# Kernel optimization log

Hardware: AMD Instinct MI355X
Metric: run time of the kernel (lower is better)

Reference implementation:

```python
import jax, jax.numpy as jnp
import numpy as np

B, S, D, NL = 512, 200, 128, 2
N_ITEMS = 50001
DH = 2 * D
DFF = 4 * D


def layer_norm(x, g, b, eps=1e-5):
    mu = x.mean(-1, keepdims=True)
    v = ((x - mu) ** 2).mean(-1, keepdims=True)
    return (x - mu) / jnp.sqrt(v + eps) * g + b


def lru_scan(h, lamb0, mask):
    # h: (B, L, DH) complex64, lamb0: (DH,) complex64, mask: (B, L) bool
    Bb, L, Dh = h.shape
    log2_L = int(np.ceil(np.log2(L)))
    lamb = lamb0.reshape(1, Dh)
    for i in range(1, log2_L + 1):
        l = 2 ** i
        h = h.reshape(Bb * L // l, l, Dh)
        m = mask.reshape(Bb * L // l, l)
        h1, h2 = h[:, : l // 2], h[:, l // 2:]
        if i > 1:
            lamb = jnp.concatenate([lamb, lamb * lamb[-1]], axis=0)  # powers lambda^1..lambda^(l/2)
        carry_gate = m[:, l // 2 - 1 : l // 2, None].astype(h.dtype)
        h2 = h2 + lamb * h1[:, -1:] * carry_gate
        h = jnp.concatenate([h1, h2], axis=1)
    return h.reshape(Bb, L, Dh)


def _forward(token_emb, emb_ln_g, emb_ln_b, params_log,
             in_wr, in_wi, in_br, in_bi, out_wr, out_wi, out_br, out_bi,
             lru_ln_g, lru_ln_b, w1, b1, w2, b2, ffn_ln_g, ffn_ln_b,
             item_seq, item_seq_len):
    mask = item_seq > 0                      # (B, S)
    x = token_emb[item_seq]                  # (B, S, D)
    x = layer_norm(x, emb_ln_g, emb_ln_b)
    seq_len = item_seq.shape[1]
    L = 2 ** int(np.ceil(np.log2(seq_len)))
    pad = L - seq_len
    x = jnp.pad(x, ((0, 0), (pad, 0), (0, 0)))        # left-pad seq to power of 2
    m = jnp.pad(mask, ((0, 0), (pad, 0)))
    n_layers = params_log.shape[0]
    for li in range(n_layers):
        pl = jnp.exp(params_log[li])                  # (3, DH): nu, theta, gamma
        nu, theta, gamma = pl[0], pl[1], pl[2]
        lamb0 = jnp.exp(jax.lax.complex(-nu, theta))  # (DH,)
        in_w = jax.lax.complex(in_wr[li], in_wi[li])
        in_b = jax.lax.complex(in_br[li], in_bi[li])
        h = (jnp.einsum('bld,hd->blh', x.astype(jnp.complex64), in_w) + in_b) * gamma
        h = lru_scan(h, lamb0, m)
        out_w = jax.lax.complex(out_wr[li], out_wi[li])
        out_b = jax.lax.complex(out_br[li], out_bi[li])
        y = (jnp.einsum('blh,dh->bld', h, out_w) + out_b).real + x
        x = layer_norm(y, lru_ln_g[li], lru_ln_b[li])
        # positionwise FFN with residual + post-LN
        hff = jax.nn.gelu(jnp.einsum('bld,fd->blf', x, w1[li]) + b1[li], approximate=False)
        x = layer_norm(jnp.einsum('blf,df->bld', hff, w2[li]) + b2[li] + x,
                       ffn_ln_g[li], ffn_ln_b[li])
    x = x[:, -seq_len:]                               # (B, S, D)
    idx = item_seq_len - 1
    return x[jnp.arange(x.shape[0]), idx]             # (B, D)


def setup_inputs() -> dict:
    key = jax.random.key(0)
    ks = jax.random.split(key, 24)
    std = 0.02
    item_seq = jax.random.randint(ks[0], (B, S), 0, N_ITEMS)
    item_seq_len = jax.random.randint(ks[1], (B,), 1, S + 1)
    # LRU diagonal init (matches torch init)
    r_min, r_max = 0.8, 0.99
    u1 = jax.random.uniform(ks[2], (NL, DH))
    u2 = jax.random.uniform(ks[3], (NL, DH))
    nu_log = jnp.log(-0.5 * jnp.log(u1 * (r_max ** 2 - r_min ** 2) + r_min ** 2))
    theta_log = jnp.log(u2 * 2.0 * np.pi)
    gamma_log = 0.5 * jnp.log(1.0 - jnp.exp(-2.0 * jnp.exp(nu_log)))
    params_log = jnp.stack([nu_log, theta_log, gamma_log], axis=1)  # (NL, 3, DH)
    rn = lambda k, sh: jax.random.normal(k, sh, dtype=jnp.float32) * std
    return {
        'token_emb': rn(ks[4], (N_ITEMS, D)),
        'emb_ln_g': jnp.ones((D,), jnp.float32), 'emb_ln_b': jnp.zeros((D,), jnp.float32),
        'params_log': params_log,
        'in_wr': rn(ks[5], (NL, DH, D)), 'in_wi': rn(ks[6], (NL, DH, D)),
        'in_br': rn(ks[7], (NL, DH)), 'in_bi': rn(ks[8], (NL, DH)),
        'out_wr': rn(ks[9], (NL, D, DH)), 'out_wi': rn(ks[10], (NL, D, DH)),
        'out_br': rn(ks[11], (NL, D)), 'out_bi': rn(ks[12], (NL, D)),
        'lru_ln_g': jnp.ones((NL, D), jnp.float32), 'lru_ln_b': jnp.zeros((NL, D), jnp.float32),
        'w1': rn(ks[13], (NL, DFF, D)), 'b1': rn(ks[14], (NL, DFF)),
        'w2': rn(ks[15], (NL, D, DFF)), 'b2': rn(ks[16], (NL, D)),
        'ffn_ln_g': jnp.ones((NL, D), jnp.float32), 'ffn_ln_b': jnp.zeros((NL, D), jnp.float32),
        'item_seq': item_seq, 'item_seq_len': item_seq_len,
    }


def reference(token_emb, emb_ln_g, emb_ln_b, params_log,
              in_wr, in_wi, in_br, in_bi, out_wr, out_wi, out_br, out_bi,
              lru_ln_g, lru_ln_b, w1, b1, w2, b2, ffn_ln_g, ffn_ln_b,
              item_seq, item_seq_len):
    return _forward(token_emb, emb_ln_g, emb_ln_b, params_log,
                    in_wr, in_wi, in_br, in_bi, out_wr, out_wi, out_br, out_bi,
                    lru_ln_g, lru_ln_b, w1, b1, w2, b2, ffn_ln_g, ffn_ln_b,
                    item_seq, item_seq_len)
```

## Files before the change

### kernel.cpp

```cpp
#include <hip/hip_runtime.h>
#include <hip/hip_bf16.h>
#include <math.h>

#define B_TOT 512
#define SEQ   200
#define D     128
#define DH    256
#define DFF   512
#define LPAD  256
#define PADL  56
#define NLAY  2
#define SST   18

typedef __attribute__((ext_vector_type(8))) short bf16x8;
typedef __attribute__((ext_vector_type(4))) float floatx4;

static __device__ inline float bf2f(ushort u) {
    union { unsigned int i; float f; } v; v.i = ((unsigned int)u) << 16; return v.f;
}
static __device__ inline ushort f2bf(float x) {
    union { float f; unsigned int i; } v; v.f = x;
    unsigned int r = (v.i + 0x7FFFu + ((v.i >> 16) & 1u)) >> 16;
    return (ushort)r;
}
static __device__ inline unsigned int pkbf(float a, float b) {
    union { __hip_bfloat162 h; unsigned int u; } v;
    v.h = __float22bfloat162_rn(make_float2(a, b));
    return v.u;
}
static __device__ inline void gld_lds16(const void* g, void* l) {
    __builtin_amdgcn_global_load_lds(
        (const __attribute__((address_space(1))) unsigned int*)g,
        (__attribute__((address_space(3))) unsigned int*)l, 16, 0, 0);
}

static __device__ inline size_t haddr(int b, int s, int k) {
    int p  = k >> 8;
    int ch = k & 255;
    int g  = ch >> 5;
    int cl = ch & 31;
    return (((((size_t)b * 8 + g) * 2 + p) * SEQ + s) * 32 + cl);
}

__global__ void setup_all_kernel(const float* __restrict__ params_log,
                                 const float* __restrict__ in_br,
                                 const float* __restrict__ in_bi,
                                 const float* __restrict__ in_wr,
                                 const float* __restrict__ in_wi,
                                 const float* __restrict__ out_wr,
                                 const float* __restrict__ out_wi,
                                 const float* __restrict__ w1,
                                 const float* __restrict__ w2,
                                 ushort* __restrict__ Winb,
                                 ushort* __restrict__ W2effb,
                                 ushort* __restrict__ w1b,
                                 ushort* __restrict__ w2b,
                                 float* __restrict__ lam_pow,
                                 float* __restrict__ scale_in,
                                 float* __restrict__ bias_in)
{
    int idx = blockIdx.x * blockDim.x + threadIdx.x;
    int li = idx >> 16;
    int e  = idx & 65535;

    {
        int gp = e >> 12, rem = e & 4095;
        int q = rem >> 3, e8 = rem & 7;
        int r = q >> 4, cs = q & 15;
        int c16 = cs ^ (r & 7);
        int n = (r < 16) ? (gp * 16 + r) : (256 + gp * 16 + (r - 16));
        int d = c16 * 8 + e8;
        float wv = (n < DH) ? in_wr[((size_t)li * DH + n) * D + d]
                            : in_wi[((size_t)li * DH + (n - DH)) * D + d];
        Winb[idx] = f2bf(wv);
    }
    {
        int k0c = e >> 13, rem = e & 8191;
        int q = rem >> 3, e8 = rem & 7;
        int r = q >> 3, cs = q & 7;
        int c16 = cs ^ (r & 7);
        int k = k0c * 64 + c16 * 8 + e8;
        float w2v = (k < DH) ? out_wr[((size_t)li * D + r) * DH + k]
                             : -out_wi[((size_t)li * D + r) * DH + (k - DH)];
        W2effb[idx] = f2bf(w2v);
    }
    {
        int row = e >> 7, col = e & 127;
        int ffc = row >> 7, rl = row & 127;
        int c16 = col >> 3, e8 = col & 7;
        int cs = c16 ^ (rl & 7);
        w1b[li * 65536 + ffc * 16384 + rl * 128 + cs * 8 + e8] = f2bf(w1[idx]);
    }
    {
        int dd2 = e >> 9, kk = e & 511;
        int ffc = kk >> 7, klc = kk & 127;
        int c16 = klc >> 3, e8 = klc & 7;
        int cs = c16 ^ (dd2 & 7);
        w2b[li * 65536 + ffc * 16384 + dd2 * 128 + cs * 8 + e8] = f2bf(w2[idx]);
    }

    if (blockIdx.x < NLAY) {
        int pli = blockIdx.x;
        int c = threadIdx.x;
        const float* pl = params_log + (size_t)pli * 3 * DH;
        float nu = expf(pl[c]);
        float th = expf(pl[DH + c]);
        float ga = expf(pl[2 * DH + c]);
        float mag = expf(-nu);
        float lr = mag * cosf(th);
        float lim = mag * sinf(th);
        float2* lp = (float2*)(lam_pow + (size_t)pli * 65536) + (size_t)c * 128;
        float pr = lr, pi = lim;
        lp[0] = make_float2(pr, pi);
        for (int k = 1; k < 128; ++k) {
            float nr = pr * lr - pi * lim;
            float ni = pr * lim + pi * lr;
            pr = nr; pi = ni;
            lp[k] = make_float2(pr, pi);
        }
        scale_in[pli * 2 * DH + c]      = ga;
        scale_in[pli * 2 * DH + DH + c] = ga;
        bias_in[pli * 2 * DH + c]       = in_br[pli * DH + c] * ga;
        bias_in[pli * 2 * DH + DH + c]  = in_bi[pli * DH + c] * ga;
    }
}

__global__ __launch_bounds__(512) void build_rowmap_kernel(
    const int* __restrict__ lenp, int Bc,
    int* __restrict__ total, int* __restrict__ rowmap)
{
    __shared__ int pre[513];
    int tid = threadIdx.x;
    int lv = (tid < Bc) ? lenp[tid] : 0;
    pre[tid + 1] = lv;
    if (tid == 0) pre[0] = 0;
    __syncthreads();
    for (int ofs = 1; ofs < 512; ofs <<= 1) {
        int v = pre[tid + 1];
        int vv = (tid + 1 > ofs) ? pre[tid + 1 - ofs] : 0;
        __syncthreads();
        pre[tid + 1] = v + vv;
        __syncthreads();
    }
    if (tid == 0) total[0] = pre[Bc];
    if (tid < Bc) {
        int base = pre[tid];
        int n = lv;
        int rb = tid * SEQ;
        for (int s = 0; s < n; ++s) rowmap[base + s] = rb + s;
    }
}

__global__ __launch_bounds__(256) void embed_ln_kernel(
    const float* __restrict__ emb, const int* __restrict__ seq,
    const int* __restrict__ lenp,
    const float* __restrict__ g, const float* __restrict__ bt,
    ushort* __restrict__ x)
{
    int row  = blockIdx.x * 4 + (threadIdx.x >> 6);
    int lane = threadIdx.x & 63;
    int b = row / SEQ, s = row - b * SEQ;
    if (s >= lenp[b]) return;
    int item = seq[row];
    float2 v = *(const float2*)(emb + (size_t)item * D + lane * 2);
    float ssum = v.x + v.y;
#pragma unroll
    for (int o = 32; o > 0; o >>= 1) ssum += __shfl_xor(ssum, o);
    float mu = ssum * (1.0f / D);
    float d0 = v.x - mu, d1 = v.y - mu;
    float vs = d0 * d0 + d1 * d1;
#pragma unroll
    for (int o = 32; o > 0; o >>= 1) vs += __shfl_xor(vs, o);
    float rstd = rsqrtf(vs * (1.0f / D) + 1e-5f);
    float2 gg = *(const float2*)(g + lane * 2);
    float2 bb = *(const float2*)(bt + lane * 2);
    unsigned int o2 = pkbf(d0 * rstd * gg.x + bb.x, d1 * rstd * gg.y + bb.y);
    *(unsigned int*)(x + (size_t)row * D + lane * 2) = o2;
}

template <bool LAST>
__global__ __launch_bounds__(512) void inproj_scan_kernel(
    const ushort* __restrict__ X, const ushort* __restrict__ Win,
    ushort* __restrict__ H, const float2* __restrict__ lamT,
    const int* __restrict__ seq, const int* __restrict__ lenp,
    const float* __restrict__ scale_in, const float* __restrict__ bias_in)
{
    __shared__ __align__(16) char smem[36864];
    __shared__ float mkf[LPAD];
    char*  Wsm = smem;
    char*  xs  = smem + 8192;
    float* stR = (float*)smem;
    float* stI = stR + LPAD * SST;
    float2* lamS = (float2*)smem;
    float2* bc   = (float2*)(smem + 16 * 130 * 8);

    int gp = blockIdx.x, b = blockIdx.y;
    int tid = threadIdx.x;
    int l = tid & 63, w = tid >> 6;
    int ct = w & 1;
    int rq = w >> 1;
    int lr = l & 15, lq = l >> 4;
    int wbase = tid & ~63;

    int c  = tid & 15;
    int tl = tid >> 4;
    int t0 = tl * 8;

    int s_b = lenp[b] - 1;
    int tile_max = s_b >> 4;
    int nrows = (tile_max + 1) * 16;
    int tb = s_b + PADL;

    const float2* myl = lamT + (size_t)(gp * 16 + c) * 128;
    float2 l14[4];
#pragma unroll
    for (int k = 0; k < 4; ++k) l14[k] = myl[k];

    if (tid < LPAD) {
        int t = tid;
        float m = 0.f;
        if (t >= PADL) m = (seq[(size_t)b * SEQ + (t - PADL)] > 0) ? 1.f : 0.f;
        mkf[t] = m;
    }

    const ushort* xrow = X + (size_t)b * SEQ * 128;
    gld_lds16(Win + (size_t)gp * 4096 + (size_t)tid * 8,
              Wsm + (size_t)wbase * 16);
#pragma unroll
    for (int it = 0; it < 4; ++it) {
        int idx = it * 512 + tid;
        if (idx < 112 * 16) {
            int r = idx >> 4, c16 = idx & 15;
            if (r < nrows) {
                uint4 v = *(const uint4*)(xrow + (size_t)r * 128 + c16 * 8);
                *(uint4*)(xs + r * 256 + ((c16 ^ (r & 7)) * 16)) = v;
            }
        }
    }
    __syncthreads();

    bf16x8 wf[4];
#pragma unroll
    for (int kk = 0; kk < 4; ++kk) {
        int ca = kk * 4 + lq;
        int wr = ct * 16 + lr;
        wf[kk] = *(const bf16x8*)(Wsm + wr * 256 + ((ca ^ (wr & 7)) * 16));
    }
    int tstart = rq ? (3 * rq + 1) : 0;
    int tcnt   = rq ? 3 : 4;
    floatx4 acc[4];
#pragma unroll
    for (int tt = 0; tt < 4; ++tt) acc[tt] = (floatx4)0.f;

    if (rq < 2) {
#pragma unroll
        for (int tt = 0; tt < 4; ++tt) {
            if (tt < tcnt && (tstart + tt) <= tile_max) {
                int t  = tstart + tt;
                int ar = t * 16 + lr;
#pragma unroll
                for (int kk = 0; kk < 4; ++kk) {
                    int ca = kk * 4 + lq;
                    bf16x8 af = *(const bf16x8*)(xs + ar * 256 + ((ca ^ (ar & 7)) * 16));
                    acc[tt] = __builtin_amdgcn_mfma_f32_16x16x32_bf16(wf[kk], af, acc[tt], 0, 0, 0);
                }
            }
        }
    }
    __syncthreads();

    if (nrows > 112) {
#pragma unroll
        for (int it = 0; it < 3; ++it) {
            int idx = it * 512 + tid;
            int r = idx >> 4, c16 = idx & 15;
            int gr = 112 + r;
            if (gr < nrows) {
                uint4 v = make_uint4(0u, 0u, 0u, 0u);
                if (gr < 200) v = *(const uint4*)(xrow + (size_t)gr * 128 + c16 * 8);
                *(uint4*)(xs + r * 256 + ((c16 ^ (r & 7)) * 16)) = v;
            }
        }
    }
    __syncthreads();

    if (rq >= 2) {
#pragma unroll
        for (int tt = 0; tt < 4; ++tt) {
            if (tt < tcnt && (tstart + tt) <= tile_max) {
                int t  = tstart + tt;
                int ar = (t - 7) * 16 + lr;
#pragma unroll
                for (int kk = 0; kk < 4; ++kk) {
                    int ca = kk * 4 + lq;
                    bf16x8 af = *(const bf16x8*)(xs + ar * 256 + ((ca ^ (ar & 7)) * 16));
                    acc[tt] = __builtin_amdgcn_mfma_f32_16x16x32_bf16(wf[kk], af, acc[tt], 0, 0, 0);
                }
            }
        }
    }
    __syncthreads();

    for (int idx = tid; idx < PADL * SST; idx += 512) { stR[idx] = 0.f; stI[idx] = 0.f; }
    {
        float4 g4 = *(const float4*)(scale_in + ct * 256 + gp * 16 + lq * 4);
        float4 b4 = *(const float4*)(bias_in  + ct * 256 + gp * 16 + lq * 4);
        float* dst = ct ? stI : stR;
#pragma unroll
        for (int tt = 0; tt < 4; ++tt) {
            if (tt < tcnt && (tstart + tt) <= tile_max) {
                int t = tstart + tt;
                int s = t * 16 + lr;
                if (s <= s_b) {
                    int pos = s + PADL;
                    dst[pos * SST + lq * 4 + 0] = acc[tt][0] * g4.x + b4.x;
                    dst[pos * SST + lq * 4 + 1] = acc[tt][1] * g4.y + b4.y;
                    dst[pos * SST + lq * 4 + 2] = acc[tt][2] * g4.z + b4.z;
                    dst[pos * SST + lq * 4 + 3] = acc[tt][3] * g4.w + b4.w;
                }
            }
        }
    }
    __syncthreads();

    float xr[8], xi[8], mf[8];
#pragma unroll
    for (int k = 0; k < 8; ++k) {
        xr[k] = stR[(t0 + k) * SST + c];
        xi[k] = stI[(t0 + k) * SST + c];
        mf[k] = mkf[t0 + k];
    }
    __syncthreads();

    {
        const char* src = (const char*)(lamT + (size_t)gp * 16 * 128);
#pragma unroll
        for (int it = 0; it < 2; ++it) {
            int idx = it * 512 + tid;
            int row = idx >> 6, c4 = idx & 63;
            *(uint4*)((char*)lamS + row * 1040 + c4 * 16) =
                *(const uint4*)(src + row * 1024 + c4 * 16);
        }
    }

    if (t0 <= tb) {
#pragma unroll
        for (int k = 0; k < 8; k += 2) {
            float sr = xr[k] * mf[k], si = xi[k] * mf[k];
            xr[k+1] += l14[0].x * sr - l14[0].y * si;
            xi[k+1] += l14[0].x * si + l14[0].y * sr;
        }
#pragma unroll
        for (int k = 1; k < 8; k += 4) {
            float sr = xr[k] * mf[k], si = xi[k] * mf[k];
            xr[k+1] += l14[0].x * sr - l14[0].y * si;
            xi[k+1] += l14[0].x * si + l14[0].y * sr;
            xr[k+2] += l14[1].x * sr - l14[1].y * si;
            xi[k+2] += l14[1].x * si + l14[1].y * sr;
        }
        {
            float sr = xr[3] * mf[3], si = xi[3] * mf[3];
#pragma unroll
            for (int j = 0; j < 4; ++j) {
                xr[4+j] += l14[j].x * sr - l14[j].y * si;
                xi[4+j] += l14[j].x * si + l14[j].y * sr;
            }
        }
    }

#pragma unroll
    for (int i = 4; i <= 8; ++i) {
        int half = 1 << (i - 1);
        if (half > tb) continue;
        int buf  = (i & 1) * 544;
        bc[buf + tl * 17 + c] = make_float2(xr[7], xi[7]);
        __syncthreads();
        int off = t0 & ((half << 1) - 1);
        if (off >= half && t0 <= tb) {
            int src = t0 - off + half - 1;
            float m = mkf[src];
            float2 sv = bc[buf + (src >> 3) * 17 + c];
            float sr = sv.x * m, si = sv.y * m;
            int e = off - half;
            const float2* lp = lamS + c * 130 + e;
#pragma unroll
            for (int k = 0; k < 8; ++k) {
                float2 lv = lp[k];
                xr[k] += lv.x * sr - lv.y * si;
                xi[k] += lv.x * si + lv.y * sr;
            }
        }
    }
    __syncthreads();

#pragma unroll
    for (int k = 0; k < 8; ++k) {
        stR[(t0 + k) * SST + c] = xr[k];
        stI[(t0 + k) * SST + c] = xi[k];
    }
    __syncthreads();

    if (LAST) {
        if (tid < 32) {
            int t = tb;
            int p = tid >> 4, cc = tid & 15;
            float v = (p ? stI : stR)[t * SST + cc];
            H[(size_t)b * 512 + p * 256 + gp * 16 + cc] = f2bf(v);
        }
    } else {
        int g  = gp >> 1;
        int hc = (gp & 1) * 16;
        ushort* baseg = H + (size_t)(b * 8 + g) * 2 * SEQ * 32 + hc;
#pragma unroll
        for (int it = 0; it < 4; ++it) {
            int idx4 = it * 512 + tid;
            if (idx4 < 2 * SEQ * 4) {
                int q  = idx4 & 3;
                int ps = idx4 >> 2;
                int p  = ps >= SEQ;
                int s  = ps - p * SEQ;
                if (s > s_b) continue;
                int t  = s + PADL;
                const float* sp = (p ? stI : stR) + t * SST + q * 4;
                float2 a = *(const float2*)(sp);
                float2 d = *(const float2*)(sp + 2);
                uint2 raw;
                raw.x = pkbf(a.x, a.y);
                raw.y = pkbf(d.x, d.y);
                *(uint2*)(baseg + (size_t)ps * 32 + q * 4) = raw;
            }
        }
    }
}

__global__ __launch_bounds__(512) void outproj_kernel(
    const ushort* __restrict__ A, const ushort* __restrict__ Wimg,
    ushort* __restrict__ Cout,
    const int* __restrict__ rowmap, const int* __restrict__ totalp,
    const float* __restrict__ e0,
    const ushort* __restrict__ res,
    const float* __restrict__ lng, const float* __restrict__ lnb)
{
    int m0 = blockIdx.x * 256;
    int total = totalp[0];
    if (m0 >= total) return;
    __shared__ __align__(16) char As[32768];
    __shared__ __align__(16) char Bs[16384];
    __shared__ float2 lnS[2][256];
    int tid = threadIdx.x;
    int l = tid & 63, w = tid >> 6;
    int chh = w >> 2;
    int rh  = w & 3;
    int lr = l & 15, lq = l >> 4;
    int wbase = tid & ~63;

    int cst = tid & 7;
    int rr  = tid >> 3;
    int sb[4], ss[4];
#pragma unroll
    for (int it = 0; it < 4; ++it) {
        int gr = m0 + it * 64 + rr;
        if (gr >= total) gr = total - 1;
        int rm = rowmap[gr];
        sb[it] = rm / SEQ; ss[it] = rm - sb[it] * SEQ;
    }

    floatx4 acc[4][4];
#pragma unroll
    for (int i = 0; i < 4; ++i)
#pragma unroll
        for (int j = 0; j < 4; ++j) acc[i][j] = (floatx4)0.f;

    for (int k0c = 0; k0c < 8; ++k0c) {
        int k0 = k0c * 64;
        {
            const ushort* img = Wimg + (size_t)k0c * 8192;
#pragma unroll
            for (int it = 0; it < 2; ++it)
                gld_lds16(img + (size_t)(it * 512 + tid) * 8,
                          Bs + (size_t)(it * 512 + wbase) * 16);
        }
#pragma unroll
        for (int it = 0; it < 4; ++it) {
            int r = it * 64 + rr;
            uint4 va = *(const uint4*)(A + haddr(sb[it], ss[it], k0 + cst * 8));
            *(uint4*)(As + r * 128 + ((cst ^ (r & 7)) * 16)) = va;
        }
        __syncthreads();
#pragma unroll
        for (int kk = 0; kk < 2; ++kk) {
            bf16x8 wf[4], af[4];
            int ca = kk * 4 + lq;
#pragma unroll
            for (int i = 0; i < 4; ++i) {
                int rb = chh * 64 + i * 16 + lr;
                wf[i] = *(const bf16x8*)(Bs + rb * 128 + ((ca ^ (rb & 7)) * 16));
                int ra = rh * 64 + i * 16 + lr;
                af[i] = *(const bf16x8*)(As + ra * 128 + ((ca ^ (ra & 7)) * 16));
            }
#pragma unroll
            for (int i = 0; i < 4; ++i)
#pragma unroll
                for (int j = 0; j < 4; ++j)
                    acc[i][j] = __builtin_amdgcn_mfma_f32_16x16x32_bf16(
                        wf[i], af[j], acc[i][j], 0, 0, 0);
        }
        __syncthreads();
    }

    int chb[4], arow[4], rmj[4];
#pragma unroll
    for (int i = 0; i < 4; ++i) chb[i] = chh * 64 + i * 16 + lq * 4;
#pragma unroll
    for (int j = 0; j < 4; ++j) {
        arow[j] = m0 + rh * 64 + j * 16 + lr;
        int rc = arow[j] < total ? arow[j] : total - 1;
        rmj[j] = rowmap[rc];
    }

    {
        float4 bias[4], gv[4], bv[4];
#pragma unroll
        for (int i = 0; i < 4; ++i) {
            bias[i] = *(const float4*)(e0 + chb[i]);
            gv[i]   = *(const float4*)(lng + chb[i]);
            bv[i]   = *(const float4*)(lnb + chb[i]);
        }
#pragma unroll
        for (int j = 0; j < 4; ++j) {
#pragma unroll
            for (int i = 0; i < 4; ++i) {
                ushort4 r4 = *(const ushort4*)(res + (size_t)rmj[j] * 128 + chb[i]);
                acc[i][j][0] += ((const float*)&bias[i])[0] + bf2f(r4.x);
                acc[i][j][1] += ((const float*)&bias[i])[1] + bf2f(r4.y);
                acc[i][j][2] += ((const float*)&bias[i])[2] + bf2f(r4.z);
                acc[i][j][3] += ((const float*)&bias[i])[3] + bf2f(r4.w);
            }
        }
#pragma unroll
        for (int j = 0; j < 4; ++j) {
            float s = 0.f, q = 0.f;
#pragma unroll
            for (int i = 0; i < 4; ++i)
#pragma unroll
                for (int reg = 0; reg < 4; ++reg) {
                    float v = acc[i][j][reg];
                    s += v; q += v * v;
                }
            s += __shfl_xor(s, 16); q += __shfl_xor(q, 16);
            s += __shfl_xor(s, 32); q += __shfl_xor(q, 32);
            if (lq == 0) lnS[chh][rh * 64 + j * 16 + lr] = make_float2(s, q);
        }
        __syncthreads();
#pragma unroll
        for (int j = 0; j < 4; ++j) {
            int rl = rh * 64 + j * 16 + lr;
            float2 s0 = lnS[0][rl], s1 = lnS[1][rl];
            float mu  = (s0.x + s1.x) * (1.0f / 128.0f);
            float var = (s0.y + s1.y) * (1.0f / 128.0f) - mu * mu;
            float rstd = rsqrtf(var + 1e-5f);
            if (arow[j] < total) {
#pragma unroll
                for (int i = 0; i < 4; ++i) {
                    uint2 u;
                    u.x = pkbf((acc[i][j][0] - mu) * rstd * ((const float*)&gv[i])[0] + ((const float*)&bv[i])[0],
                               (acc[i][j][1] - mu) * rstd * ((const float*)&gv[i])[1] + ((const float*)&bv[i])[1]);
                    u.y = pkbf((acc[i][j][2] - mu) * rstd * ((const float*)&gv[i])[2] + ((const float*)&bv[i])[2],
                               (acc[i][j][3] - mu) * rstd * ((const float*)&gv[i])[3] + ((const float*)&bv[i])[3]);
                    *(uint2*)(Cout + (size_t)rmj[j] * 128 + chb[i]) = u;
                }
            }
        }
    }
}

__global__ __launch_bounds__(512) void outproj_last_kernel(
    const ushort* __restrict__ Hc, const ushort* __restrict__ Wimg,
    ushort* __restrict__ xc, int Bc,
    const float* __restrict__ e0,
    const ushort* __restrict__ Xres, const int* __restrict__ lenp,
    const float* __restrict__ lng, const float* __restrict__ lnb)
{
    __shared__ __align__(16) char As[32768];
    __shared__ __align__(16) char Bs[16384];
    __shared__ float2 lnS[2][256];
    int tid = threadIdx.x;
    int l = tid & 63, w = tid >> 6;
    int chh = w >> 2;
    int rh  = w & 3;
    int lr = l & 15, lq = l >> 4;
    int m0 = blockIdx.x * 256;
    int wbase = tid & ~63;

    int cst = tid & 7;
    int rr  = tid >> 3;

    floatx4 acc[4][4];
#pragma unroll
    for (int i = 0; i < 4; ++i)
#pragma unroll
        for (int j = 0; j < 4; ++j) acc[i][j] = (floatx4)0.f;

    for (int k0c = 0; k0c < 8; ++k0c) {
        int k0 = k0c * 64;
        {
            const ushort* img = Wimg + (size_t)k0c * 8192;
#pragma unroll
            for (int it = 0; it < 2; ++it)
                gld_lds16(img + (size_t)(it * 512 + tid) * 8,
                          Bs + (size_t)(it * 512 + wbase) * 16);
        }
#pragma unroll
        for (int it = 0; it < 4; ++it) {
            int r = it * 64 + rr;
            int gr = m0 + r; if (gr >= Bc) gr = Bc - 1;
            uint4 va = *(const uint4*)(Hc + (size_t)gr * 512 + k0 + cst * 8);
            *(uint4*)(As + r * 128 + ((cst ^ (r & 7)) * 16)) = va;
        }
        __syncthreads();
#pragma unroll
        for (int kk = 0; kk < 2; ++kk) {
            bf16x8 wf[4], af[4];
            int ca = kk * 4 + lq;
#pragma unroll
            for (int i = 0; i < 4; ++i) {
                int rb = chh * 64 + i * 16 + lr;
                wf[i] = *(const bf16x8*)(Bs + rb * 128 + ((ca ^ (rb & 7)) * 16));
                int ra = rh * 64 + i * 16 + lr;
                af[i] = *(const bf16x8*)(As + ra * 128 + ((ca ^ (ra & 7)) * 16));
            }
#pragma unroll
            for (int i = 0; i < 4; ++i)
#pragma unroll
                for (int j = 0; j < 4; ++j)
                    acc[i][j] = __builtin_amdgcn_mfma_f32_16x16x32_bf16(
                        wf[i], af[j], acc[i][j], 0, 0, 0);
        }
        __syncthreads();
    }

    int chb[4], arow[4];
#pragma unroll
    for (int i = 0; i < 4; ++i) chb[i] = chh * 64 + i * 16 + lq * 4;
#pragma unroll
    for (int j = 0; j < 4; ++j) arow[j] = m0 + rh * 64 + j * 16 + lr;

    {
        float4 bias[4], gv[4], bv[4];
#pragma unroll
        for (int i = 0; i < 4; ++i) {
            bias[i] = *(const float4*)(e0 + chb[i]);
            gv[i]   = *(const float4*)(lng + chb[i]);
            bv[i]   = *(const float4*)(lnb + chb[i]);
        }
#pragma unroll
        for (int j = 0; j < 4; ++j) {
            int br = arow[j] < Bc ? arow[j] : Bc - 1;
            int sb_ = lenp[br] - 1;
            const ushort* rbase = Xres + ((size_t)br * SEQ + sb_) * 128;
#pragma unroll
            for (int i = 0; i < 4; ++i) {
                ushort4 r4 = *(const ushort4*)(rbase + chb[i]);
                acc[i][j][0] += ((const float*)&bias[i])[0] + bf2f(r4.x);
                acc[i][j][1] += ((const float*)&bias[i])[1] + bf2f(r4.y);
                acc[i][j][2] += ((const float*)&bias[i])[2] + bf2f(r4.z);
                acc[i][j][3] += ((const float*)&bias[i])[3] + bf2f(r4.w);
            }
        }
#pragma unroll
        for (int j = 0; j < 4; ++j) {
            float s = 0.f, q = 0.f;
#pragma unroll
            for (int i = 0; i < 4; ++i)
#pragma unroll
                for (int reg = 0; reg < 4; ++reg) {
                    float v = acc[i][j][reg];
                    s += v; q += v * v;
                }
            s += __shfl_xor(s, 16); q += __shfl_xor(q, 16);
            s += __shfl_xor(s, 32); q += __shfl_xor(q, 32);
            if (lq == 0) lnS[chh][rh * 64 + j * 16 + lr] = make_float2(s, q);
        }
        __syncthreads();
#pragma unroll
        for (int j = 0; j < 4; ++j) {
            int rl = rh * 64 + j * 16 + lr;
            float2 s0 = lnS[0][rl], s1 = lnS[1][rl];
            float mu  = (s0.x + s1.x) * (1.0f / 128.0f);
            float var = (s0.y + s1.y) * (1.0f / 128.0f) - mu * mu;
            float rstd = rsqrtf(var + 1e-5f);
            if (arow[j] < Bc) {
#pragma unroll
                for (int i = 0; i < 4; ++i) {
                    uint2 u;
                    u.x = pkbf((acc[i][j][0] - mu) * rstd * ((const float*)&gv[i])[0] + ((const float*)&bv[i])[0],
                               (acc[i][j][1] - mu) * rstd * ((const float*)&gv[i])[1] + ((const float*)&bv[i])[1]);
                    u.y = pkbf((acc[i][j][2] - mu) * rstd * ((const float*)&gv[i])[2] + ((const float*)&bv[i])[2],
                               (acc[i][j][3] - mu) * rstd * ((const float*)&gv[i])[3] + ((const float*)&bv[i])[3]);
                    *(uint2*)(xc + (size_t)arow[j] * 128 + chb[i]) = u;
                }
            }
        }
    }
}

__global__ __launch_bounds__(256) void ffn_fused_kernel(
    ushort* __restrict__ X, const ushort* __restrict__ W1,
    const ushort* __restrict__ W2,
    const float* __restrict__ b1, const float* __restrict__ b2,
    const float* __restrict__ lng, const float* __restrict__ lnb,
    int Mtot, const int* __restrict__ rowmap, const int* __restrict__ totalp)
{
    int m0 = blockIdx.x * 64;
    int total = totalp ? totalp[0] : Mtot;
    if (m0 >= total) return;
    __shared__ __align__(16) char Bs[32768];
    __shared__ ushort Ps[64 * 136];
    __shared__ float2 lnS[2][64];
    int tid = threadIdx.x;
    int l = tid & 63, w = tid >> 6;
    int chh = w >> 1, rh = w & 1;
    int lr = l & 15, lq = l >> 4;
    int wbase = tid & ~63;

    int arow[2], rmrow[2];
#pragma unroll
    for (int j = 0; j < 2; ++j) {
        arow[j] = m0 + rh * 32 + j * 16 + lr;
        int rc = arow[j] < total ? arow[j] : total - 1;
        rmrow[j] = rowmap ? rowmap[rc] : rc;
    }

    bf16x8 af_x[8];
#pragma unroll
    for (int j = 0; j < 2; ++j)
#pragma unroll
        for (int kk2 = 0; kk2 < 4; ++kk2) {
            int k = kk2 * 32 + lq * 8;
            af_x[(j << 2) | kk2] = *(const bf16x8*)(X + (size_t)rmrow[j] * 128 + k);
        }

    floatx4 acc2[4][2];
#pragma unroll
    for (int i = 0; i < 4; ++i)
#pragma unroll
        for (int j = 0; j < 2; ++j) acc2[i][j] = (floatx4)0.f;

    for (int ffc = 0; ffc < 4; ++ffc) {
        if (ffc) __syncthreads();
        {
            const ushort* img = W1 + (size_t)ffc * 16384;
#pragma unroll
            for (int it = 0; it < 8; ++it)
                gld_lds16(img + (size_t)(it * 256 + tid) * 8,
                          Bs + (size_t)(it * 256 + wbase) * 16);
        }
        __syncthreads();

        floatx4 acc1[4][2];
#pragma unroll
        for (int i = 0; i < 4; ++i)
#pragma unroll
            for (int j = 0; j < 2; ++j) acc1[i][j] = (floatx4)0.f;
#pragma unroll
        for (int kk2 = 0; kk2 < 4; ++kk2) {
            int ca = kk2 * 4 + lq;
            bf16x8 wf[4];
#pragma unroll
            for (int i = 0; i < 4; ++i) {
                int rb = chh * 64 + i * 16 + lr;
                wf[i] = *(const bf16x8*)(Bs + rb * 256 + ((ca ^ (rb & 7)) * 16));
            }
#pragma unroll
            for (int i = 0; i < 4; ++i)
#pragma unroll
                for (int j = 0; j < 2; ++j)
                    acc1[i][j] = __builtin_amdgcn_mfma_f32_16x16x32_bf16(
                        wf[i], af_x[(j << 2) | kk2], acc1[i][j], 0, 0, 0);
        }

#pragma unroll
        for (int j = 0; j < 2; ++j) {
            int rowl = rh * 32 + j * 16 + lr;
#pragma unroll
            for (int i = 0; i < 4; ++i) {
                int ch0 = chh * 64 + i * 16 + lq * 4;
                float4 bv = *(const float4*)(b1 + ffc * 128 + ch0);
                float g0, g1, g2, g3, v;
                v = acc1[i][j][0] + bv.x; g0 = 0.5f * v * (1.0f + erff(v * 0.70710678118654752f));
                v = acc1[i][j][1] + bv.y; g1 = 0.5f * v * (1.0f + erff(v * 0.70710678118654752f));
                v = acc1[i][j][2] + bv.z; g2 = 0.5f * v * (1.0f + erff(v * 0.70710678118654752f));
                v = acc1[i][j][3] + bv.w; g3 = 0.5f * v * (1.0f + erff(v * 0.70710678118654752f));
                uint2 u; u.x = pkbf(g0, g1); u.y = pkbf(g2, g3);
                *(uint2*)(Ps + rowl * 136 + ch0) = u;
            }
        }
        __syncthreads();

        {
            const ushort* img = W2 + (size_t)ffc * 16384;
#pragma unroll
            for (int it = 0; it < 8; ++it)
                gld_lds16(img + (size_t)(it * 256 + tid) * 8,
                          Bs + (size_t)(it * 256 + wbase) * 16);
        }
        __syncthreads();

#pragma unroll
        for (int kk2 = 0; kk2 < 4; ++kk2) {
            int ca = kk2 * 4 + lq;
            bf16x8 wf[4], af[2];
#pragma unroll
            for (int i = 0; i < 4; ++i) {
                int rb = chh * 64 + i * 16 + lr;
                wf[i] = *(const bf16x8*)(Bs + rb * 256 + ((ca ^ (rb & 7)) * 16));
            }
#pragma unroll
            for (int j = 0; j < 2; ++j) {
                int rowl = rh * 32 + j * 16 + lr;
                af[j] = *(const bf16x8*)(Ps + rowl * 136 + kk2 * 32 + lq * 8);
            }
#pragma unroll
            for (int i = 0; i < 4; ++i)
#pragma unroll
                for (int j = 0; j < 2; ++j)
                    acc2[i][j] = __builtin_amdgcn_mfma_f32_16x16x32_bf16(
                        wf[i], af[j], acc2[i][j], 0, 0, 0);
        }
    }

    int chb[4];
#pragma unroll
    for (int i = 0; i < 4; ++i) chb[i] = chh * 64 + i * 16 + lq * 4;

    float4 bias[4], gv[4], bv[4];
#pragma unroll
    for (int i = 0; i < 4; ++i) {
        bias[i] = *(const float4*)(b2 + chb[i]);
        gv[i]   = *(const float4*)(lng + chb[i]);
        bv[i]   = *(const float4*)(lnb + chb[i]);
    }
#pragma unroll
    for (int j = 0; j < 2; ++j) {
#pragma unroll
        for (int i = 0; i < 4; ++i) {
            ushort4 r4 = *(const ushort4*)(X + (size_t)rmrow[j] * 128 + chb[i]);
            acc2[i][j][0] += ((const float*)&bias[i])[0] + bf2f(r4.x);
            acc2[i][j][1] += ((const float*)&bias[i])[1] + bf2f(r4.y);
            acc2[i][j][2] += ((const float*)&bias[i])[2] + bf2f(r4.z);
            acc2[i][j][3] += ((const float*)&bias[i])[3] + bf2f(r4.w);
        }
    }
#pragma unroll
    for (int j = 0; j < 2; ++j) {
        float s = 0.f, q = 0.f;
#pragma unroll
        for (int i = 0; i < 4; ++i)
#pragma unroll
            for (int reg = 0; reg < 4; ++reg) {
                float v = acc2[i][j][reg];
                s += v; q += v * v;
            }
        s += __shfl_xor(s, 16); q += __shfl_xor(q, 16);
        s += __shfl_xor(s, 32); q += __shfl_xor(q, 32);
        if (lq == 0) lnS[chh][rh * 32 + j * 16 + lr] = make_float2(s, q);
    }
    __syncthreads();
#pragma unroll
    for (int j = 0; j < 2; ++j) {
        int rl = rh * 32 + j * 16 + lr;
        float2 s0 = lnS[0][rl], s1 = lnS[1][rl];
        float mu  = (s0.x + s1.x) * (1.0f / 128.0f);
        float var = (s0.y + s1.y) * (1.0f / 128.0f) - mu * mu;
        float rstd = rsqrtf(var + 1e-5f);
        if (arow[j] < total) {
#pragma unroll
            for (int i = 0; i < 4; ++i) {
                uint2 u;
                u.x = pkbf((acc2[i][j][0] - mu) * rstd * ((const float*)&gv[i])[0] + ((const float*)&bv[i])[0],
                           (acc2[i][j][1] - mu) * rstd * ((const float*)&gv[i])[1] + ((const float*)&bv[i])[1]);
                u.y = pkbf((acc2[i][j][2] - mu) * rstd * ((const float*)&gv[i])[2] + ((const float*)&bv[i])[2],
                           (acc2[i][j][3] - mu) * rstd * ((const float*)&gv[i])[3] + ((const float*)&bv[i])[3]);
                *(uint2*)(X + (size_t)rmrow[j] * 128 + chb[i]) = u;
            }
        }
    }
}

__global__ void gather_final_kernel(const ushort* __restrict__ xc,
                                    float* __restrict__ out, int b0, int Bc)
{
    int i = blockIdx.x * 256 + threadIdx.x;
    if (i >= Bc * D) return;
    out[(size_t)b0 * D + i] = bf2f(xc[i]);
}

extern "C" void kernel_launch(void* const* d_in, const int* in_sizes, int n_in,
                              void* d_out, int out_size, void* d_ws, size_t ws_size,
                              hipStream_t stream)
{
    const float* token_emb  = (const float*)d_in[0];
    const float* emb_ln_g   = (const float*)d_in[1];
    const float* emb_ln_b   = (const float*)d_in[2];
    const float* params_log = (const float*)d_in[3];
    const float* in_wr      = (const float*)d_in[4];
    const float* in_wi      = (const float*)d_in[5];
    const float* in_br      = (const float*)d_in[6];
    const float* in_bi      = (const float*)d_in[7];
    const float* out_wr     = (const float*)d_in[8];
    const float* out_wi     = (const float*)d_in[9];
    const float* out_br     = (const float*)d_in[10];
    const float* lru_ln_g   = (const float*)d_in[12];
    const float* lru_ln_b   = (const float*)d_in[13];
    const float* w1         = (const float*)d_in[14];
    const float* b1         = (const float*)d_in[15];
    const float* w2         = (const float*)d_in[16];
    const float* b2         = (const float*)d_in[17];
    const float* ffn_ln_g   = (const float*)d_in[18];
    const float* ffn_ln_b   = (const float*)d_in[19];
    const int*   item_seq   = (const int*)d_in[20];
    const int*   item_seq_len = (const int*)d_in[21];
    float* out = (float*)d_out;

    char* ws = (char*)d_ws;
    ushort* Winb   = (ushort*)ws;                      ws += NLAY * 65536 * 2;
    ushort* W2effb = (ushort*)ws;                      ws += NLAY * 65536 * 2;
    ushort* w1b    = (ushort*)ws;                      ws += NLAY * 65536 * 2;
    ushort* w2b    = (ushort*)ws;                      ws += NLAY * 65536 * 2;
    float* lam_pow = (float*)ws;                       ws += NLAY * 65536 * 4;
    float* scale_in = (float*)ws;                      ws += NLAY * 512 * 4;
    float* bias_in  = (float*)ws;                      ws += NLAY * 512 * 4;
    size_t table_bytes = (size_t)(ws - (char*)d_ws);

    int Bc = B_TOT;
    while (Bc > 32) {
        size_t need = table_bytes
                    + (size_t)Bc * SEQ * (D * 2 + 2 * DH * 2)
                    + (size_t)(Bc * SEQ + 8) * 4 + 1024;
        if (need <= ws_size) break;
        Bc >>= 1;
    }
    ushort* xb = (ushort*)ws;                          ws += (size_t)Bc * SEQ * D * 2;
    ushort* hb = (ushort*)ws;                          ws += (size_t)Bc * SEQ * 2 * DH * 2;
    int* totalp = (int*)ws;                            ws += 8 * 4;
    int* rowmap = (int*)ws;
    ushort* Hc = hb;
    ushort* xc = hb + (size_t)Bc * 512;

    setup_all_kernel<<<NLAY * 65536 / 256, 256, 0, stream>>>(
        params_log, in_br, in_bi, in_wr, in_wi, out_wr, out_wi, w1, w2,
        Winb, W2effb, w1b, w2b, lam_pow, scale_in, bias_in);

    for (int b0 = 0; b0 < B_TOT; b0 += Bc) {
        int M = Bc * SEQ;
        const int* lenp = item_seq_len + b0;
        build_rowmap_kernel<<<1, 512, 0, stream>>>(lenp, Bc, totalp, rowmap);
        embed_ln_kernel<<<M / 4, 256, 0, stream>>>(
            token_emb, item_seq + (size_t)b0 * SEQ, lenp,
            emb_ln_g, emb_ln_b, xb);

        for (int li = 0; li < NLAY; ++li) {
            if (li < NLAY - 1) {
                inproj_scan_kernel<false><<<dim3(16, Bc), 512, 0, stream>>>(
                    xb, Winb + (size_t)li * 65536, hb,
                    (const float2*)(lam_pow + (size_t)li * 65536),
                    item_seq + (size_t)b0 * SEQ, lenp,
                    scale_in + li * 512, bias_in + li * 512);
                outproj_kernel<<<dim3(M / 256), 512, 0, stream>>>(
                    hb, W2effb + (size_t)li * 65536, xb, rowmap, totalp,
                    out_br + li * D, xb,
                    lru_ln_g + li * D, lru_ln_b + li * D);
                ffn_fused_kernel<<<dim3(M / 64), 256, 0, stream>>>(
                    xb, w1b + (size_t)li * 65536, w2b + (size_t)li * 65536,
                    b1 + li * DFF, b2 + li * D,
                    ffn_ln_g + li * D, ffn_ln_b + li * D, M, rowmap, totalp);
            } else {
                inproj_scan_kernel<true><<<dim3(16, Bc), 512, 0, stream>>>(
                    xb, Winb + (size_t)li * 65536, Hc,
                    (const float2*)(lam_pow + (size_t)li * 65536),
                    item_seq + (size_t)b0 * SEQ, lenp,
                    scale_in + li * 512, bias_in + li * 512);
                outproj_last_kernel<<<dim3((Bc + 255) / 256), 512, 0, stream>>>(
                    Hc, W2effb + (size_t)li * 65536, xc, Bc,
                    out_br + li * D, xb, lenp,
                    lru_ln_g + li * D, lru_ln_b + li * D);
                ffn_fused_kernel<<<dim3((Bc + 63) / 64), 256, 0, stream>>>(
                    xc, w1b + (size_t)li * 65536, w2b + (size_t)li * 65536,
                    b1 + li * DFF, b2 + li * D,
                    ffn_ln_g + li * D, ffn_ln_b + li * D, Bc,
                    (const int*)0, (const int*)0);
            }
        }
        gather_final_kernel<<<(Bc * D + 255) / 256, 256, 0, stream>>>(
            xc, out, b0, Bc);
    }
}
```

Baseline: 438.5 us.

## Restructure LRU scan carry propagation with shuffles and deferred carry accumulation

Reworks the in-projection + scan kernel. Levels 4-5 of the scan are done with wave shuffles instead of shared-memory broadcasts and barriers. Only each thread's last element is updated at every level, while an accumulated carry is applied to the other seven elements once at the end. This removes the lambda-power table staging in LDS, and the X tile is loaded with direct global-to-LDS copies. Only the rows that are needed are written back, which trims LDS traffic, barriers and per-level FLOPs, at the cost of more complex indexing and a changed floating-point summation order.

```diff
diff --git a/kernel.cpp b/kernel.cpp
--- a/kernel.cpp
+++ b/kernel.cpp
@@ -191,8 +191,7 @@
     char*  xs  = smem + 8192;
     float* stR = (float*)smem;
     float* stI = stR + LPAD * SST;
-    float2* lamS = (float2*)smem;
-    float2* bc   = (float2*)(smem + 16 * 130 * 8);
+    float2* bc   = (float2*)(smem + 16640);
 
     int gp = blockIdx.x, b = blockIdx.y;
     int tid = threadIdx.x;
@@ -210,11 +209,22 @@
     int tile_max = s_b >> 4;
     int nrows = (tile_max + 1) * 16;
     int tb = s_b + PADL;
+    bool activeT = (t0 <= tb);
+
+    const ushort* xrow = X + (size_t)b * SEQ * 128;
+    gld_lds16(Win + (size_t)gp * 4096 + (size_t)tid * 8,
+              Wsm + (size_t)wbase * 16);
+    int nrA = nrows < 112 ? nrows : 112;
+#pragma unroll
+    for (int it = 0; it < 4; ++it) {
+        int rbase = it * 32 + w * 4;
+        int r = rbase + lq;
+        int cs = lr ^ (r & 7);
+        if (r < nrA)
+            gld_lds16(xrow + (size_t)r * 128 + cs * 8, xs + rbase * 256);
+    }
 
     const float2* myl = lamT + (size_t)(gp * 16 + c) * 128;
-    float2 l14[4];
-#pragma unroll
-    for (int k = 0; k < 4; ++k) l14[k] = myl[k];
 
     if (tid < LPAD) {
         int t = tid;
@@ -222,21 +232,6 @@
         if (t >= PADL) m = (seq[(size_t)b * SEQ + (t - PADL)] > 0) ? 1.f : 0.f;
         mkf[t] = m;
     }
-
-    const ushort* xrow = X + (size_t)b * SEQ * 128;
-    gld_lds16(Win + (size_t)gp * 4096 + (size_t)tid * 8,
-              Wsm + (size_t)wbase * 16);
-#pragma unroll
-    for (int it = 0; it < 4; ++it) {
-        int idx = it * 512 + tid;
-        if (idx < 112 * 16) {
-            int r = idx >> 4, c16 = idx & 15;
-            if (r < nrows) {
-                uint4 v = *(const uint4*)(xrow + (size_t)r * 128 + c16 * 8);
-                *(uint4*)(xs + r * 256 + ((c16 ^ (r & 7)) * 16)) = v;
-            }
-        }
-    }
     __syncthreads();
 
     bf16x8 wf[4];
@@ -270,16 +265,15 @@
     __syncthreads();
 
     if (nrows > 112) {
+        int nrB = nrows < 200 ? nrows : 200;
 #pragma unroll
         for (int it = 0; it < 3; ++it) {
-            int idx = it * 512 + tid;
-            int r = idx >> 4, c16 = idx & 15;
-            int gr = 112 + r;
-            if (gr < nrows) {
-                uint4 v = make_uint4(0u, 0u, 0u, 0u);
-                if (gr < 200) v = *(const uint4*)(xrow + (size_t)gr * 128 + c16 * 8);
-                *(uint4*)(xs + r * 256 + ((c16 ^ (r & 7)) * 16)) = v;
-            }
+            int rbase = it * 32 + w * 4;
+            int rl_ = rbase + lq;
+            int gr = 112 + rl_;
+            int cs = lr ^ (rl_ & 7);
+            if (gr < nrB)
+                gld_lds16(xrow + (size_t)gr * 128 + cs * 8, xs + rbase * 256);
         }
     }
     __syncthreads();
@@ -300,6 +294,22 @@
         }
     }
     __syncthreads();
+
+    float2 l14[4];
+#pragma unroll
+    for (int k = 0; k < 4; ++k) l14[k] = myl[k];
+    float2 myl9 = myl[8];
+    float2 lam_e[3];
+#pragma unroll
+    for (int i = 0; i < 3; ++i) {
+        int half = 32 << i;
+        int off = t0 & ((half << 1) - 1);
+        int e = off - half;
+        lam_e[i] = myl[e < 0 ? 0 : e];
+    }
+    float2 l7;
+    l7.x = l14[3].x * l14[2].x - l14[3].y * l14[2].y;
+    l7.y = l14[3].x * l14[2].y + l14[3].y * l14[2].x;
 
     for (int idx = tid; idx < PADL * SST; idx += 512) { stR[idx] = 0.f; stI[idx] = 0.f; }
     {
@@ -323,27 +333,17 @@
     }
     __syncthreads();
 
-    float xr[8], xi[8], mf[8];
-#pragma unroll
-    for (int k = 0; k < 8; ++k) {
-        xr[k] = stR[(t0 + k) * SST + c];
-        xi[k] = stI[(t0 + k) * SST + c];
-        mf[k] = mkf[t0 + k];
-    }
-    __syncthreads();
-
-    {
-        const char* src = (const char*)(lamT + (size_t)gp * 16 * 128);
-#pragma unroll
-        for (int it = 0; it < 2; ++it) {
-            int idx = it * 512 + tid;
-            int row = idx >> 6, c4 = idx & 63;
-            *(uint4*)((char*)lamS + row * 1040 + c4 * 16) =
-                *(const uint4*)(src + row * 1024 + c4 * 16);
-        }
-    }
-
-    if (t0 <= tb) {
+    float xr[8], xi[8];
+    if (activeT) {
+#pragma unroll
+        for (int k = 0; k < 8; ++k) {
+            xr[k] = stR[(t0 + k) * SST + c];
+            xi[k] = stI[(t0 + k) * SST + c];
+        }
+        float mf[8];
+#pragma unroll
+        for (int k = 0; k < 8; ++k) mf[k] = mkf[t0 + k];
+
 #pragma unroll
         for (int k = 0; k < 8; k += 2) {
             float sr = xr[k] * mf[k], si = xi[k] * mf[k];
@@ -366,37 +366,96 @@
                 xi[4+j] += l14[j].x * si + l14[j].y * sr;
             }
         }
-    }
-
-#pragma unroll
-    for (int i = 4; i <= 8; ++i) {
+    } else {
+        xr[7] = 0.f; xi[7] = 0.f;
+    }
+
+    float Ctr = 0.f, Cti = 0.f;
+
+    {
+        float svx = __shfl_xor(xr[7], 16);
+        float svy = __shfl_xor(xi[7], 16);
+        if (activeT && (tl & 1)) {
+            float m = mkf[t0 - 1];
+            float sr = svx * m, si = svy * m;
+            float cr = l14[0].x * sr - l14[0].y * si;
+            float ci = l14[0].x * si + l14[0].y * sr;
+            Ctr += cr; Cti += ci;
+            xr[7] += l7.x * cr - l7.y * ci;
+            xi[7] += l7.x * ci + l7.y * cr;
+        }
+    }
+    {
+        float svx = __shfl(xr[7], 16 + c);
+        float svy = __shfl(xi[7], 16 + c);
+        if (activeT && (tl & 2)) {
+            float m = mkf[(t0 & ~31) + 15];
+            float2 le = (tl & 1) ? myl9 : l14[0];
+            float sr = svx * m, si = svy * m;
+            float cr = le.x * sr - le.y * si;
+            float ci = le.x * si + le.y * sr;
+            Ctr += cr; Cti += ci;
+            xr[7] += l7.x * cr - l7.y * ci;
+            xi[7] += l7.x * ci + l7.y * cr;
+        }
+    }
+    __syncthreads();
+
+#pragma unroll
+    for (int i = 6; i <= 8; ++i) {
         int half = 1 << (i - 1);
         if (half > tb) continue;
-        int buf  = (i & 1) * 544;
-        bc[buf + tl * 17 + c] = make_float2(xr[7], xi[7]);
+        int buf = (i & 1) * 544;
+        if (activeT) bc[buf + tl * 17 + c] = make_float2(xr[7], xi[7]);
         __syncthreads();
         int off = t0 & ((half << 1) - 1);
-        if (off >= half && t0 <= tb) {
-            int src = t0 - off + half - 1;
-            float m = mkf[src];
-            float2 sv = bc[buf + (src >> 3) * 17 + c];
+        if (activeT && off >= half) {
+            int srcp = t0 - off + half - 1;
+            float m = mkf[srcp];
+            float2 sv = bc[buf + (srcp >> 3) * 17 + c];
+            float2 le = lam_e[i - 6];
             float sr = sv.x * m, si = sv.y * m;
-            int e = off - half;
-            const float2* lp = lamS + c * 130 + e;
+            float cr = le.x * sr - le.y * si;
+            float ci = le.x * si + le.y * sr;
+            Ctr += cr; Cti += ci;
+            xr[7] += l7.x * cr - l7.y * ci;
+            xi[7] += l7.x * ci + l7.y * cr;
+        }
+    }
+    __syncthreads();
+
+    if (activeT && (!LAST || (unsigned)(tb - t0) < 7u)) {
+        float2 l5, l6;
+        l5.x = l14[3].x * l14[0].x - l14[3].y * l14[0].y;
+        l5.y = l14[3].x * l14[0].y + l14[3].y * l14[0].x;
+        l6.x = l14[3].x * l14[1].x - l14[3].y * l14[1].y;
+        l6.y = l14[3].x * l14[1].y + l14[3].y * l14[1].x;
+        xr[0] += Ctr;                               xi[0] += Cti;
+        xr[1] += l14[0].x*Ctr - l14[0].y*Cti;       xi[1] += l14[0].x*Cti + l14[0].y*Ctr;
+        xr[2] += l14[1].x*Ctr - l14[1].y*Cti;       xi[2] += l14[1].x*Cti + l14[1].y*Ctr;
+        xr[3] += l14[2].x*Ctr - l14[2].y*Cti;       xi[3] += l14[2].x*Cti + l14[2].y*Ctr;
+        xr[4] += l14[3].x*Ctr - l14[3].y*Cti;       xi[4] += l14[3].x*Cti + l14[3].y*Ctr;
+        xr[5] += l5.x*Ctr - l5.y*Cti;               xi[5] += l5.x*Cti + l5.y*Ctr;
+        xr[6] += l6.x*Ctr - l6.y*Cti;               xi[6] += l6.x*Cti + l6.y*Ctr;
+    }
+
+    if (LAST) {
+        if (activeT && (unsigned)(tb - t0) < 8u) {
+#pragma unroll
+            for (int k = 0; k < 8; ++k)
+                if (t0 + k == tb) {
+                    stR[tb * SST + c] = xr[k];
+                    stI[tb * SST + c] = xi[k];
+                }
+        }
+    } else {
+        if (activeT && tl >= 7) {
 #pragma unroll
             for (int k = 0; k < 8; ++k) {
-                float2 lv = lp[k];
-                xr[k] += lv.x * sr - lv.y * si;
-                xi[k] += lv.x * si + lv.y * sr;
-            }
-        }
-    }
-    __syncthreads();
-
-#pragma unroll
-    for (int k = 0; k < 8; ++k) {
-        stR[(t0 + k) * SST + c] = xr[k];
-        stI[(t0 + k) * SST + c] = xi[k];
+                stR[(t0 + k) * SST + c] = xr[k];
+                stI[(t0 + k) * SST + c] = xi[k];
+            }
+        }
     }
     __syncthreads();
 
```

After: 444.8 us. About the same (+1.4%).
